# Performance work log

Measured on AMD Instinct MI355X. Metric: run time of the kernel, lower is better.

Reference implementation:

```python
import jax, jax.numpy as jnp
import numpy as np

CIN = 28
HID1, HID2 = 64, 64
U_IDX, V_IDX = 11, 12
MU_U, SD_U = 0.02, 0.15
MU_V, SD_V = -0.01, 0.12


def setup_inputs() -> dict:
    key = jax.random.key(0)
    ks = jax.random.split(key, 18)
    B, T, H, W = 8, 8, 128, 128
    s = 0.05
    f32 = jnp.float32
    d = {
        "x": jax.random.normal(ks[0], (B, T, CIN, H, W), f32),
        # reduce: Conv2d(Cin, 24, 1)
        "W_red": jax.random.normal(ks[1], (24, CIN), f32) * s,
        "b_red": jnp.zeros((24,), f32),
        # l1: LSTMCell(24, HID1) + Conv2d(HID1, HID1, 1)
        "Wih1": jax.random.normal(ks[2], (4 * HID1, 24), f32) * s,
        "Whh1": jax.random.normal(ks[3], (4 * HID1, HID1), f32) * s,
        "bih1": jnp.zeros((4 * HID1,), f32),
        "bhh1": jnp.zeros((4 * HID1,), f32),
        "Wc1": jax.random.normal(ks[4], (HID1, HID1), f32) * s,
        "bc1": jnp.zeros((HID1,), f32),
        # l2: LSTMCell(HID1, HID2) + Conv2d(HID2, HID2, 1)
        "Wih2": jax.random.normal(ks[5], (4 * HID2, HID1), f32) * s,
        "Whh2": jax.random.normal(ks[6], (4 * HID2, HID2), f32) * s,
        "bih2": jnp.zeros((4 * HID2,), f32),
        "bhh2": jnp.zeros((4 * HID2,), f32),
        "Wc2": jax.random.normal(ks[7], (HID2, HID2), f32) * s,
        "bc2": jnp.zeros((HID2,), f32),
        # head: Conv2d(HID2, 1, 1)
        "W_head": jax.random.normal(ks[8], (1, HID2), f32) * s,
        "b_head": jnp.zeros((1,), f32),
    }
    return d


def _lstm_cell(flat, h, c, Wih, Whh, bih, bhh):
    # PyTorch LSTMCell gate order: i, f, g, o
    g = flat @ Wih.T + bih + h @ Whh.T + bhh
    i, f, gg, o = jnp.split(g, 4, axis=1)
    c = jax.nn.sigmoid(f) * c + jax.nn.sigmoid(i) * jnp.tanh(gg)
    h = jax.nn.sigmoid(o) * jnp.tanh(c)
    return h, c


def _conv1x1(x, W, b):
    # x: [B,C,H,W], W: [O,C]
    return jnp.einsum('bchw,oc->bohw', x, W) + b[None, :, None, None]


def reference(x, W_red, b_red, Wih1, Whh1, bih1, bhh1, Wc1, bc1,
              Wih2, Whh2, bih2, bhh2, Wc2, bc2, W_head, b_head):
    B, T, C, H, W = x.shape
    N = B * H * W
    # de-normalize u/v channels for every timestep (dropout p=0 -> identity)
    x = x.at[:, :, U_IDX].set(x[:, :, U_IDX] * SD_U + MU_U)
    x = x.at[:, :, V_IDX].set(x[:, :, V_IDX] * SD_V + MU_V)

    def step(carry, frame):
        h1, c1, h2, c2 = carry
        inp = _conv1x1(frame, W_red, b_red)                 # [B,24,H,W]
        flat1 = inp.transpose(0, 2, 3, 1).reshape(N, 24)    # pixel-wise rows
        h1, c1 = _lstm_cell(flat1, h1, c1, Wih1, Whh1, bih1, bhh1)
        h1_map = h1.reshape(B, H, W, HID1).transpose(0, 3, 1, 2)
        o1 = _conv1x1(h1_map, Wc1, bc1)                     # [B,HID1,H,W]
        flat2 = o1.transpose(0, 2, 3, 1).reshape(N, HID1)
        h2, c2 = _lstm_cell(flat2, h2, c2, Wih2, Whh2, bih2, bhh2)
        return (h1, c1, h2, c2), None

    z1 = jnp.zeros((N, HID1), x.dtype)
    z2 = jnp.zeros((N, HID2), x.dtype)
    xs = jnp.transpose(x, (1, 0, 2, 3, 4))                  # [T,B,C,H,W]
    (h1, c1, h2, c2), _ = jax.lax.scan(step, (z1, z1, z2, z2), xs)
    # only the last o2 is used by the head
    h2_map = h2.reshape(B, H, W, HID2).transpose(0, 3, 1, 2)
    o2 = _conv1x1(h2_map, Wc2, bc2)                         # [B,HID2,H,W]
    out = _conv1x1(o2, W_head, b_head)                      # [B,1,H,W]
    return out[:, 0]                                        # squeeze(1) -> [B,H,W]
```

## Files before the change

kernel.cpp:

```cpp
#include <hip/hip_runtime.h>

typedef _Float16 f16;
typedef _Float16 f16x2 __attribute__((ext_vector_type(2)));
typedef _Float16 f16x4 __attribute__((ext_vector_type(4)));
typedef _Float16 f16x8 __attribute__((ext_vector_type(8)));
typedef float f32x4 __attribute__((ext_vector_type(4)));

#define CIN 28
#define TT 8
#define HW 16384

#define S_SIG  (-1.44269504088896341f)
#define S_TANH ( 2.88539008177792681f)

#define WS_WX    0
#define WS_WHH1  16384
#define WS_W21   49152
#define WS_WHH2  81920
#define WS_BX    114688
#define WS_B2    115712
#define WS_WH    116736
#define WS_BH    116992

__device__ __forceinline__ float lstm_act(float gi, float gf, float gg, float go,
                                          float& c) {
  const float Ei = __builtin_amdgcn_exp2f(gi);
  const float Ef = __builtin_amdgcn_exp2f(gf);
  const float Eg = __builtin_amdgcn_exp2f(gg);
  const float Eo = __builtin_amdgcn_exp2f(go);
  const float pig = (1.f + Ei) * (1.f + Eg);
  const float pf  = 1.f + Ef;
  const float r3  = __builtin_amdgcn_rcpf(pig * pf);
  const float t1  = (Eg - 1.f) * pf;
  const float cn  = r3 * __builtin_fmaf(pig, c, t1);
  c = cn;
  const float Ec  = __builtin_amdgcn_exp2f(cn * S_TANH);
  const float roc = __builtin_amdgcn_rcpf((1.f + Eo) * (1.f + Ec));
  return (Ec - 1.f) * roc;
}

__global__ __launch_bounds__(64) void prep_kernel(
    const float* __restrict__ W_red, const float* __restrict__ b_red,
    const float* __restrict__ Wih1, const float* __restrict__ Whh1,
    const float* __restrict__ bih1, const float* __restrict__ bhh1,
    const float* __restrict__ Wc1,  const float* __restrict__ bc1,
    const float* __restrict__ Wih2, const float* __restrict__ Whh2,
    const float* __restrict__ bih2, const float* __restrict__ bhh2,
    const float* __restrict__ Wc2,  const float* __restrict__ bc2,
    const float* __restrict__ W_head, const float* __restrict__ b_head,
    unsigned char* __restrict__ ws)
{
  const int g = blockIdx.x;
  const int k = threadIdx.x;
  f16* WxH   = (f16*)(ws + WS_WX);
  f16* Whh1H = (f16*)(ws + WS_WHH1);
  f16* W21H  = (f16*)(ws + WS_W21);
  f16* Whh2H = (f16*)(ws + WS_WHH2);
  float* BX  = (float*)(ws + WS_BX);
  float* B2  = (float*)(ws + WS_B2);
  float* WHp = (float*)(ws + WS_WH);
  float* BHp = (float*)(ws + WS_BH);

  const int gate = g >> 6;
  const int col  = g & 63;
  const int pr = (col >> 3) * 32 + (col & 1) * 16 + ((col >> 1) & 3) * 4 + gate;

  const float sc = (gate == 2) ? S_TANH : S_SIG;

  float wxv = 0.f;
  if (k < CIN) {
    float s = 0.f;
    for (int r = 0; r < 24; ++r) s += Wih1[g*24 + r] * W_red[r*28 + k];
    wxv = s;
  }
  const float wx11 = __shfl(wxv, 11, 64);
  const float wx12 = __shfl(wxv, 12, 64);
  if (k == 11) wxv *= 0.15f;
  if (k == 12) wxv *= 0.12f;
  if (k < 32) WxH[pr*32 + k] = (f16)(wxv * sc);

  Whh1H[pr*64 + k] = (f16)(Whh1[g*64 + k] * sc);
  Whh2H[pr*64 + k] = (f16)(Whh2[g*64 + k] * sc);

  {
    float s = 0.f;
    for (int m = 0; m < 64; ++m) s += Wih2[g*64 + m] * Wc1[m*64 + k];
    W21H[pr*64 + k] = (f16)(s * sc);
  }

  if (k == 0) {
    float bx = bih1[g] + bhh1[g];
    for (int r = 0; r < 24; ++r) bx += Wih1[g*24 + r] * b_red[r];
    bx += wx11 * 0.02f + wx12 * (-0.01f);
    BX[pr] = bx * sc;
    float b2v = bih2[g] + bhh2[g];
    for (int m = 0; m < 64; ++m) b2v += Wih2[g*64 + m] * bc1[m];
    B2[pr] = b2v * sc;
  }
  if (g == 0) {
    float s = 0.f;
    for (int m = 0; m < 64; ++m) s += W_head[m] * Wc2[m*64 + k];
    WHp[k] = s;
    if (k == 0) {
      float s2 = b_head[0];
      for (int m = 0; m < 64; ++m) s2 += W_head[m] * bc2[m];
      BHp[0] = s2;
    }
  }
}

__global__ __launch_bounds__(512, 4)
void convlstm_main(
    const float* __restrict__ x, const unsigned char* __restrict__ ws,
    float* __restrict__ out)
{
  __shared__ __align__(16) f16 xs[2][64 * 40];
  __shared__ __align__(16) f16 h1buf[2][64 * 72];
  __shared__ __align__(16) f16 h2buf[2][64 * 72];

  const int tid  = threadIdx.x;
  const int lane = tid & 63;
  const int wv   = tid >> 6;
  const int cl   = lane & 15;
  const int qd   = lane >> 4;

  const f16* WxG   = (const f16*)(ws + WS_WX);
  const f16* Whh1G = (const f16*)(ws + WS_WHH1);
  const f16* W21G  = (const f16*)(ws + WS_W21);
  const f16* Whh2G = (const f16*)(ws + WS_WHH2);
  const float* BX  = (const float*)(ws + WS_BX);
  const float* B2  = (const float*)(ws + WS_B2);

  f16x8 wx[2];
  f16x8 whh1[2][2], w21[2][2], whh2[2][2];
  f32x4 bxq[2], b2q[2];
#pragma unroll
  for (int rt = 0; rt < 2; ++rt) {
    const int pr = wv*32 + rt*16 + cl;
    wx[rt]      = *(const f16x8*)(WxG + pr*32 + qd*8);
    whh1[rt][0] = *(const f16x8*)(Whh1G + pr*64 + qd*8);
    whh1[rt][1] = *(const f16x8*)(Whh1G + pr*64 + 32 + qd*8);
    w21[rt][0]  = *(const f16x8*)(W21G  + pr*64 + qd*8);
    w21[rt][1]  = *(const f16x8*)(W21G  + pr*64 + 32 + qd*8);
    whh2[rt][0] = *(const f16x8*)(Whh2G + pr*64 + qd*8);
    whh2[rt][1] = *(const f16x8*)(Whh2G + pr*64 + 32 + qd*8);
    bxq[rt] = *(const f32x4*)(BX + wv*32 + rt*16 + 4*qd);
    b2q[rt] = *(const f32x4*)(B2 + wv*32 + rt*16 + 4*qd);
  }

  {
    unsigned* z1 = (unsigned*)&h1buf[0][0];
    unsigned* z2 = (unsigned*)&h2buf[0][0];
#pragma unroll
    for (int i = tid; i < 2304; i += 512) { z1[i] = 0u; z2[i] = 0u; }
  }

  const int gpix = blockIdx.x * 64;
  const float* xb = x + (size_t)(gpix >> 14) * (TT * CIN * HW) + (gpix & (HW - 1));

  const int sp = lane;
  const int cg = wv;

  {
    f16x4 v;
#pragma unroll
    for (int j = 0; j < 4; ++j) {
      const int ch = cg*4 + j;
      v[j] = (ch < CIN) ? (f16)xb[ch*HW + sp] : (f16)0.f;
    }
    *(f16x4*)(&xs[0][sp*40 + cg*4]) = v;
  }
  __syncthreads();

  float c1s[4][2];
  float c2s[4][2];
#pragma unroll
  for (int a = 0; a < 4; ++a)
#pragma unroll
    for (int b = 0; b < 2; ++b) { c1s[a][b] = 0.f; c2s[a][b] = 0.f; }

#pragma unroll 1
  for (int t = 0; t < TT; ++t) {
    f16x4 xrv;
    if (t + 1 < TT) {
      const float* xt = xb + (size_t)(t + 1) * (CIN * HW);
#pragma unroll
      for (int j = 0; j < 4; ++j) {
        const int ch = cg*4 + j;
        xrv[j] = (ch < CIN) ? (f16)xt[ch*HW + sp] : (f16)0.f;
      }
    }

    const f16* xsr = xs[t & 1];
    const f16* h1r = h1buf[t & 1];
    const f16* h2r = h2buf[t & 1];
    f16* h1w = h1buf[(t + 1) & 1];
    f16* h2w = h2buf[(t + 1) & 1];

#pragma unroll
    for (int mb = 0; mb < 4; ++mb) {
      const int p = 16*mb + cl;
      const f16x8 ax  = *(const f16x8*)(xsr + p*40 + qd*8);
      const f16x8 ah0 = *(const f16x8*)(h1r + p*72 + qd*8);
      const f16x8 ah1 = *(const f16x8*)(h1r + p*72 + 32 + qd*8);
      float hn[2];
#pragma unroll
      for (int rt = 0; rt < 2; ++rt) {
        f32x4 acc;
        acc = __builtin_amdgcn_mfma_f32_16x16x32_f16(whh1[rt][0], ah0, bxq[rt], 0, 0, 0);
        acc = __builtin_amdgcn_mfma_f32_16x16x32_f16(whh1[rt][1], ah1, acc, 0, 0, 0);
        acc = __builtin_amdgcn_mfma_f32_16x16x32_f16(wx[rt],      ax,  acc, 0, 0, 0);
        hn[rt] = lstm_act(acc[0], acc[1], acc[2], acc[3], c1s[mb][rt]);
      }
      f16x2 hv; hv[0] = (f16)hn[0]; hv[1] = (f16)hn[1];
      *(f16x2*)(h1w + p*72 + 8*wv + 2*qd) = hv;
    }
    __syncthreads();

    if (t + 1 < TT) {
      f16* xsw = xs[(t + 1) & 1];
      *(f16x4*)(xsw + sp*40 + cg*4) = xrv;
    }

#pragma unroll
    for (int mb = 0; mb < 4; ++mb) {
      const int p = 16*mb + cl;
      const f16x8 an0 = *(const f16x8*)(h1w + p*72 + qd*8);
      const f16x8 an1 = *(const f16x8*)(h1w + p*72 + 32 + qd*8);
      const f16x8 a20 = *(const f16x8*)(h2r + p*72 + qd*8);
      const f16x8 a21 = *(const f16x8*)(h2r + p*72 + 32 + qd*8);
      float hn[2];
#pragma unroll
      for (int rt = 0; rt < 2; ++rt) {
        f32x4 acc;
        acc = __builtin_amdgcn_mfma_f32_16x16x32_f16(w21[rt][0],  an0, b2q[rt], 0, 0, 0);
        acc = __builtin_amdgcn_mfma_f32_16x16x32_f16(w21[rt][1],  an1, acc, 0, 0, 0);
        acc = __builtin_amdgcn_mfma_f32_16x16x32_f16(whh2[rt][0], a20, acc, 0, 0, 0);
        acc = __builtin_amdgcn_mfma_f32_16x16x32_f16(whh2[rt][1], a21, acc, 0, 0, 0);
        hn[rt] = lstm_act(acc[0], acc[1], acc[2], acc[3], c2s[mb][rt]);
      }
      f16x2 hv; hv[0] = (f16)hn[0]; hv[1] = (f16)hn[1];
      *(f16x2*)(h2w + p*72 + 8*wv + 2*qd) = hv;
    }
    __syncthreads();
  }

  if (tid < 64) {
    const float* wh = (const float*)(ws + WS_WH);
    const f16* row = &h2buf[0][tid * 72];
    float s = *((const float*)(ws + WS_BH));
#pragma unroll
    for (int k = 0; k < 64; ++k) s += (float)row[k] * wh[k];
    out[gpix + tid] = s;
  }
}

extern "C" void kernel_launch(void* const* d_in, const int* in_sizes, int n_in,
                              void* d_out, int out_size, void* d_ws, size_t ws_size,
                              hipStream_t stream) {
  const float* x      = (const float*)d_in[0];
  const float* W_red  = (const float*)d_in[1];
  const float* b_red  = (const float*)d_in[2];
  const float* Wih1   = (const float*)d_in[3];
  const float* Whh1   = (const float*)d_in[4];
  const float* bih1   = (const float*)d_in[5];
  const float* bhh1   = (const float*)d_in[6];
  const float* Wc1    = (const float*)d_in[7];
  const float* bc1    = (const float*)d_in[8];
  const float* Wih2   = (const float*)d_in[9];
  const float* Whh2   = (const float*)d_in[10];
  const float* bih2   = (const float*)d_in[11];
  const float* bhh2   = (const float*)d_in[12];
  const float* Wc2    = (const float*)d_in[13];
  const float* bc2    = (const float*)d_in[14];
  const float* W_head = (const float*)d_in[15];
  const float* b_head = (const float*)d_in[16];

  prep_kernel<<<256, 64, 0, stream>>>(W_red, b_red, Wih1, Whh1, bih1, bhh1,
                                      Wc1, bc1, Wih2, Whh2, bih2, bhh2,
                                      Wc2, bc2, W_head, b_head,
                                      (unsigned char*)d_ws);
  convlstm_main<<<2048, 512, 0, stream>>>(x, (const unsigned char*)d_ws,
                                          (float*)d_out);
}
```

Measured before the change: 386.2 us.

## Split gate rows across 16 waves per block with bias staged in LDS

Doubles the block to 1024 threads (16 waves) so that each wave owns one 16-row gate tile instead of two. This halves the per-thread weight registers and MFMA chains, which is meant to raise latency hiding and occupancy per CU. The gate-row permutation in the prep kernel is changed to match, bias vectors are moved from registers into LDS, and the x-frame staging is redistributed across the larger block. In exchange, each barrier now synchronises more waves, and each thread does less work between barriers.

```diff
diff --git a/kernel.cpp b/kernel.cpp
--- a/kernel.cpp
+++ b/kernel.cpp
@@ -2,7 +2,6 @@
 
 typedef _Float16 f16;
 typedef _Float16 f16x2 __attribute__((ext_vector_type(2)));
-typedef _Float16 f16x4 __attribute__((ext_vector_type(4)));
 typedef _Float16 f16x8 __attribute__((ext_vector_type(8)));
 typedef float f32x4 __attribute__((ext_vector_type(4)));
 
@@ -63,7 +62,7 @@
 
   const int gate = g >> 6;
   const int col  = g & 63;
-  const int pr = (col >> 3) * 32 + (col & 1) * 16 + ((col >> 1) & 3) * 4 + gate;
+  const int pr = 16 * (col >> 2) + 4 * (col & 3) + gate;
 
   const float sc = (gate == 2) ? S_TANH : S_SIG;
 
@@ -109,7 +108,7 @@
   }
 }
 
-__global__ __launch_bounds__(512, 4)
+__global__ __launch_bounds__(1024, 8)
 void convlstm_main(
     const float* __restrict__ x, const unsigned char* __restrict__ ws,
     float* __restrict__ out)
@@ -117,6 +116,7 @@
   __shared__ __align__(16) f16 xs[2][64 * 40];
   __shared__ __align__(16) f16 h1buf[2][64 * 72];
   __shared__ __align__(16) f16 h2buf[2][64 * 72];
+  __shared__ __align__(16) float biasLds[512];
 
   const int tid  = threadIdx.x;
   const int lane = tid & 63;
@@ -131,64 +131,56 @@
   const float* BX  = (const float*)(ws + WS_BX);
   const float* B2  = (const float*)(ws + WS_B2);
 
-  f16x8 wx[2];
-  f16x8 whh1[2][2], w21[2][2], whh2[2][2];
-  f32x4 bxq[2], b2q[2];
-#pragma unroll
-  for (int rt = 0; rt < 2; ++rt) {
-    const int pr = wv*32 + rt*16 + cl;
-    wx[rt]      = *(const f16x8*)(WxG + pr*32 + qd*8);
-    whh1[rt][0] = *(const f16x8*)(Whh1G + pr*64 + qd*8);
-    whh1[rt][1] = *(const f16x8*)(Whh1G + pr*64 + 32 + qd*8);
-    w21[rt][0]  = *(const f16x8*)(W21G  + pr*64 + qd*8);
-    w21[rt][1]  = *(const f16x8*)(W21G  + pr*64 + 32 + qd*8);
-    whh2[rt][0] = *(const f16x8*)(Whh2G + pr*64 + qd*8);
-    whh2[rt][1] = *(const f16x8*)(Whh2G + pr*64 + 32 + qd*8);
-    bxq[rt] = *(const f32x4*)(BX + wv*32 + rt*16 + 4*qd);
-    b2q[rt] = *(const f32x4*)(B2 + wv*32 + rt*16 + 4*qd);
-  }
+  f16x8 wx, whh1k0, whh1k1, w21k0, w21k1, whh2k0, whh2k1;
+  {
+    const int pr = wv*16 + cl;
+    wx     = *(const f16x8*)(WxG   + pr*32 + qd*8);
+    whh1k0 = *(const f16x8*)(Whh1G + pr*64 + qd*8);
+    whh1k1 = *(const f16x8*)(Whh1G + pr*64 + 32 + qd*8);
+    w21k0  = *(const f16x8*)(W21G  + pr*64 + qd*8);
+    w21k1  = *(const f16x8*)(W21G  + pr*64 + 32 + qd*8);
+    whh2k0 = *(const f16x8*)(Whh2G + pr*64 + qd*8);
+    whh2k1 = *(const f16x8*)(Whh2G + pr*64 + 32 + qd*8);
+  }
+
+  if (tid < 256)       biasLds[tid]       = BX[tid];
+  else if (tid < 512)  biasLds[tid]       = B2[tid - 256];
 
   {
     unsigned* z1 = (unsigned*)&h1buf[0][0];
     unsigned* z2 = (unsigned*)&h2buf[0][0];
-#pragma unroll
-    for (int i = tid; i < 2304; i += 512) { z1[i] = 0u; z2[i] = 0u; }
+    for (int i = tid; i < 2304; i += 1024) { z1[i] = 0u; z2[i] = 0u; }
   }
 
   const int gpix = blockIdx.x * 64;
   const float* xb = x + (size_t)(gpix >> 14) * (TT * CIN * HW) + (gpix & (HW - 1));
 
-  const int sp = lane;
-  const int cg = wv;
-
-  {
-    f16x4 v;
-#pragma unroll
-    for (int j = 0; j < 4; ++j) {
-      const int ch = cg*4 + j;
-      v[j] = (ch < CIN) ? (f16)xb[ch*HW + sp] : (f16)0.f;
-    }
-    *(f16x4*)(&xs[0][sp*40 + cg*4]) = v;
+  const int pxl = (lane & 15) + 16 * (wv & 3);
+  const int chp = 4 * (wv >> 2) + (lane >> 4);
+
+  {
+    f16x2 v;
+    const int c0 = chp*2, c1 = chp*2 + 1;
+    v[0] = (c0 < CIN) ? (f16)xb[c0*HW + pxl] : (f16)0.f;
+    v[1] = (c1 < CIN) ? (f16)xb[c1*HW + pxl] : (f16)0.f;
+    *(f16x2*)(&xs[0][pxl*40 + chp*2]) = v;
   }
   __syncthreads();
 
-  float c1s[4][2];
-  float c2s[4][2];
-#pragma unroll
-  for (int a = 0; a < 4; ++a)
-#pragma unroll
-    for (int b = 0; b < 2; ++b) { c1s[a][b] = 0.f; c2s[a][b] = 0.f; }
+  float c1s[4], c2s[4];
+#pragma unroll
+  for (int a = 0; a < 4; ++a) { c1s[a] = 0.f; c2s[a] = 0.f; }
+
+  const int bofs = wv*16 + 4*qd;
 
 #pragma unroll 1
   for (int t = 0; t < TT; ++t) {
-    f16x4 xrv;
+    f16x2 xrv;
     if (t + 1 < TT) {
       const float* xt = xb + (size_t)(t + 1) * (CIN * HW);
-#pragma unroll
-      for (int j = 0; j < 4; ++j) {
-        const int ch = cg*4 + j;
-        xrv[j] = (ch < CIN) ? (f16)xt[ch*HW + sp] : (f16)0.f;
-      }
+      const int c0 = chp*2, c1 = chp*2 + 1;
+      xrv[0] = (c0 < CIN) ? (f16)xt[c0*HW + pxl] : (f16)0.f;
+      xrv[1] = (c1 < CIN) ? (f16)xt[c1*HW + pxl] : (f16)0.f;
     }
 
     const f16* xsr = xs[t & 1];
@@ -197,31 +189,27 @@
     f16* h1w = h1buf[(t + 1) & 1];
     f16* h2w = h2buf[(t + 1) & 1];
 
+    const f32x4 bxq = *(const f32x4*)(&biasLds[bofs]);
 #pragma unroll
     for (int mb = 0; mb < 4; ++mb) {
       const int p = 16*mb + cl;
       const f16x8 ax  = *(const f16x8*)(xsr + p*40 + qd*8);
       const f16x8 ah0 = *(const f16x8*)(h1r + p*72 + qd*8);
       const f16x8 ah1 = *(const f16x8*)(h1r + p*72 + 32 + qd*8);
-      float hn[2];
-#pragma unroll
-      for (int rt = 0; rt < 2; ++rt) {
-        f32x4 acc;
-        acc = __builtin_amdgcn_mfma_f32_16x16x32_f16(whh1[rt][0], ah0, bxq[rt], 0, 0, 0);
-        acc = __builtin_amdgcn_mfma_f32_16x16x32_f16(whh1[rt][1], ah1, acc, 0, 0, 0);
-        acc = __builtin_amdgcn_mfma_f32_16x16x32_f16(wx[rt],      ax,  acc, 0, 0, 0);
-        hn[rt] = lstm_act(acc[0], acc[1], acc[2], acc[3], c1s[mb][rt]);
-      }
-      f16x2 hv; hv[0] = (f16)hn[0]; hv[1] = (f16)hn[1];
-      *(f16x2*)(h1w + p*72 + 8*wv + 2*qd) = hv;
+      f32x4 acc;
+      acc = __builtin_amdgcn_mfma_f32_16x16x32_f16(whh1k0, ah0, bxq, 0, 0, 0);
+      acc = __builtin_amdgcn_mfma_f32_16x16x32_f16(whh1k1, ah1, acc, 0, 0, 0);
+      acc = __builtin_amdgcn_mfma_f32_16x16x32_f16(wx,     ax,  acc, 0, 0, 0);
+      const float hn = lstm_act(acc[0], acc[1], acc[2], acc[3], c1s[mb]);
+      h1w[p*72 + 4*wv + qd] = (f16)hn;
     }
     __syncthreads();
 
     if (t + 1 < TT) {
-      f16* xsw = xs[(t + 1) & 1];
-      *(f16x4*)(xsw + sp*40 + cg*4) = xrv;
-    }
-
+      *(f16x2*)(xs[(t + 1) & 1] + pxl*40 + chp*2) = xrv;
+    }
+
+    const f32x4 b2q = *(const f32x4*)(&biasLds[256 + bofs]);
 #pragma unroll
     for (int mb = 0; mb < 4; ++mb) {
       const int p = 16*mb + cl;
@@ -229,18 +217,13 @@
       const f16x8 an1 = *(const f16x8*)(h1w + p*72 + 32 + qd*8);
       const f16x8 a20 = *(const f16x8*)(h2r + p*72 + qd*8);
       const f16x8 a21 = *(const f16x8*)(h2r + p*72 + 32 + qd*8);
-      float hn[2];
-#pragma unroll
-      for (int rt = 0; rt < 2; ++rt) {
-        f32x4 acc;
-        acc = __builtin_amdgcn_mfma_f32_16x16x32_f16(w21[rt][0],  an0, b2q[rt], 0, 0, 0);
-        acc = __builtin_amdgcn_mfma_f32_16x16x32_f16(w21[rt][1],  an1, acc, 0, 0, 0);
-        acc = __builtin_amdgcn_mfma_f32_16x16x32_f16(whh2[rt][0], a20, acc, 0, 0, 0);
-        acc = __builtin_amdgcn_mfma_f32_16x16x32_f16(whh2[rt][1], a21, acc, 0, 0, 0);
-        hn[rt] = lstm_act(acc[0], acc[1], acc[2], acc[3], c2s[mb][rt]);
-      }
-      f16x2 hv; hv[0] = (f16)hn[0]; hv[1] = (f16)hn[1];
-      *(f16x2*)(h2w + p*72 + 8*wv + 2*qd) = hv;
+      f32x4 acc;
+      acc = __builtin_amdgcn_mfma_f32_16x16x32_f16(w21k0,  an0, b2q, 0, 0, 0);
+      acc = __builtin_amdgcn_mfma_f32_16x16x32_f16(w21k1,  an1, acc, 0, 0, 0);
+      acc = __builtin_amdgcn_mfma_f32_16x16x32_f16(whh2k0, a20, acc, 0, 0, 0);
+      acc = __builtin_amdgcn_mfma_f32_16x16x32_f16(whh2k1, a21, acc, 0, 0, 0);
+      const float hn = lstm_act(acc[0], acc[1], acc[2], acc[3], c2s[mb]);
+      h2w[p*72 + 4*wv + qd] = (f16)hn;
     }
     __syncthreads();
   }
@@ -280,6 +263,6 @@
                                       Wc1, bc1, Wih2, Whh2, bih2, bhh2,
                                       Wc2, bc2, W_head, b_head,
                                       (unsigned char*)d_ws);
-  convlstm_main<<<2048, 512, 0, stream>>>(x, (const unsigned char*)d_ws,
-                                          (float*)d_out);
-}
+  convlstm_main<<<2048, 1024, 0, stream>>>(x, (const unsigned char*)d_ws,
+                                           (float*)d_out);
+}
```

After: 391.9 us. Within noise of the previous version (+1.5%).
